# Kernel optimization log

Hardware: AMD Instinct MI355X
Metric: run time of the kernel (lower is better)

Reference implementation:

```python
import jax, jax.numpy as jnp
import numpy as np

IN_CH = 512
MID = max(IN_CH // 8, 1)


def setup_inputs() -> dict:
    key = jax.random.key(0)
    ks = jax.random.split(key, 8)
    B, C, H, W = 4, IN_CH, 64, 64
    s = 0.05
    x = jax.random.normal(ks[0], (B, C, H, W), dtype=jnp.float32)
    wq = jax.random.normal(ks[1], (MID, C), dtype=jnp.float32) * s
    bq = jnp.zeros((MID,), dtype=jnp.float32)
    wk = jax.random.normal(ks[2], (MID, C), dtype=jnp.float32) * s
    bk = jnp.zeros((MID,), dtype=jnp.float32)
    wv = jax.random.normal(ks[3], (C, C), dtype=jnp.float32) * s
    bv = jnp.zeros((C,), dtype=jnp.float32)
    alpha = jnp.ones((1,), dtype=jnp.float32) * 0.5  # nonzero so attention path is exercised
    return {"x": x, "wq": wq, "bq": bq, "wk": wk, "bk": bk, "wv": wv, "bv": bv, "alpha": alpha}


def reference(x, wq, bq, wk, bk, wv, bv, alpha):
    B, C, H, W = x.shape
    N = H * W
    xf = x.reshape(B, C, N)  # [B, C, N]
    # 1x1 convs == per-position channel GEMMs
    q = jnp.einsum('mc,bcn->bnm', wq, xf) + bq  # [B, N, mid]
    k = jnp.einsum('mc,bcn->bmn', wk, xf) + bk[None, :, None]  # [B, mid, N]
    v = jnp.einsum('dc,bcn->bdn', wv, xf) + bv[None, :, None]  # [B, C, N]
    attn = jax.nn.softmax(jnp.einsum('bnm,bmk->bnk', q, k), axis=-1)  # [B, N, N]
    out = jnp.einsum('bdn,bkn->bdk', v, attn)  # v @ attn^T -> [B, C, N]
    out = out.reshape(B, C, H, W)
    return alpha * out + x
```

## Files before the change

### kernel.cpp

```cpp
#include <hip/hip_runtime.h>

#define BB 4
#define CD 512
#define NP 4096
#define MID 64

typedef _Float16 half8 __attribute__((ext_vector_type(8)));
typedef _Float16 half4 __attribute__((ext_vector_type(4)));
typedef float floatx4 __attribute__((ext_vector_type(4)));

#define LOG2E 1.4426950408889634f

__global__ __launch_bounds__(256) void prep_w(
    const float* __restrict__ wq, const float* __restrict__ wk,
    const float* __restrict__ wv, const float* __restrict__ bq,
    const float* __restrict__ bk, const float* __restrict__ bv,
    _Float16* __restrict__ w_h, float* __restrict__ bias) {
  int idx = blockIdx.x * 256 + threadIdx.x;
  for (int i = idx; i < 640 * 512; i += gridDim.x * 256) {
    int r = i >> 9, c = i & 511;
    float v = (r < 64) ? wq[(r << 9) + c] * LOG2E
            : (r < 128) ? wk[((r - 64) << 9) + c]
                        : wv[((r - 128) << 9) + c];
    w_h[i] = (_Float16)v;
  }
  if (idx < 640) {
    float v = (idx < 64) ? bq[idx] * LOG2E
            : (idx < 128) ? bk[idx - 64]
                          : bv[idx - 128];
    bias[idx] = v;
  }
}

__global__ __launch_bounds__(256) void transpose_x(const float* __restrict__ x,
                                                   _Float16* __restrict__ xt) {
  __shared__ float tile[64][65];
  int b = blockIdx.z, c0 = blockIdx.y * 64, n0 = blockIdx.x * 64;
  int t = threadIdx.x;
  const float* xb = x + (size_t)b * CD * NP;
#pragma unroll
  for (int k = 0; k < 16; k++) {
    int cl = k * 4 + (t >> 6);
    int nl = t & 63;
    tile[cl][nl] = xb[(size_t)(c0 + cl) * NP + n0 + nl];
  }
  __syncthreads();
  _Float16* xtb = xt + ((size_t)b * NP + n0) * CD + c0;
#pragma unroll
  for (int k = 0; k < 2; k++) {
    int nl = k * 32 + (t >> 3);
    int cl = (t & 7) * 8;
    half8 pk;
#pragma unroll
    for (int i = 0; i < 8; i++) pk[i] = (_Float16)tile[cl + i][nl];
    *(half8*)(xtb + (size_t)nl * CD + cl) = pk;
  }
}

__global__ __launch_bounds__(256, 2) void proj_qkv(
    const _Float16* __restrict__ w_h, const float* __restrict__ bias,
    const _Float16* __restrict__ xt, _Float16* __restrict__ q_h,
    _Float16* __restrict__ k_h, _Float16* __restrict__ v_h) {
  __shared__ _Float16 xls[64 * 512];
  int t = threadIdx.x, w = t >> 6, lane = t & 63;
  int col = lane & 15, quad = lane >> 4;
  int rbh = blockIdx.x, nb = blockIdx.y, b = blockIdx.z;
  int n0 = nb * 64;
  const _Float16* xtb = xt + ((size_t)b * NP + n0) * CD;
#pragma unroll
  for (int j = 0; j < 16; j++) {
    int u = t + j * 256;
    int row = u >> 6, un = u & 63;
    *(half8*)(xls + row * 512 + ((un ^ (row & 7)) << 3)) =
        *(const half8*)(xtb + (size_t)row * CD + un * 8);
  }
  __syncthreads();

  int rw = rbh * 320 + w * 80;
  floatx4 acc[5][4] = {};
  for (int c = 0; c < CD; c += 32) {
    int cu = c >> 3;
    half8 a[5], bf[4];
#pragma unroll
    for (int i = 0; i < 5; i++)
      a[i] = *(const half8*)(w_h + (size_t)(rw + i * 16 + col) * CD + c + quad * 8);
#pragma unroll
    for (int j = 0; j < 4; j++) {
      int row = j * 16 + col;
      bf[j] = *(const half8*)(xls + row * 512 + (((cu + quad) ^ (row & 7)) << 3));
    }
#pragma unroll
    for (int i = 0; i < 5; i++)
#pragma unroll
      for (int j = 0; j < 4; j++)
        acc[i][j] = __builtin_amdgcn_mfma_f32_16x16x32_f16(a[i], bf[j], acc[i][j], 0, 0, 0);
  }

#pragma unroll
  for (int i = 0; i < 5; i++) {
    int r0 = rw + i * 16;
    float bi[4];
#pragma unroll
    for (int rr = 0; rr < 4; rr++) bi[rr] = bias[r0 + quad * 4 + rr];
    if (r0 < 128) {
      _Float16* dst = (r0 < 64 ? q_h + (size_t)b * NP * MID + r0
                               : k_h + (size_t)b * NP * MID + (r0 - 64));
#pragma unroll
      for (int j = 0; j < 4; j++) {
        int n = n0 + j * 16 + col;
        half4 pk;
#pragma unroll
        for (int rr = 0; rr < 4; rr++) pk[rr] = (_Float16)(acc[i][j][rr] + bi[rr]);
        *(half4*)(dst + (size_t)n * MID + quad * 4) = pk;
      }
    } else {
      int dbase = r0 - 128 + quad * 4;
#pragma unroll
      for (int j = 0; j < 4; j++) {
        int n = n0 + j * 16 + col;
#pragma unroll
        for (int rr = 0; rr < 4; rr++)
          v_h[((size_t)b * CD + dbase + rr) * NP + n] =
              (_Float16)(acc[i][j][rr] + bi[rr]);
      }
    }
  }
}

__global__ __launch_bounds__(256) void rowmax(const _Float16* __restrict__ q_h,
                                              const _Float16* __restrict__ k_h,
                                              float* __restrict__ M) {
  int qb = blockIdx.x, b = blockIdx.y;
  int t = threadIdx.x, w = t >> 6, lane = t & 63;
  int col = lane & 15, quad = lane >> 4;
  int q0 = qb * 32;
  const _Float16* qp = q_h + ((size_t)b * NP + q0) * MID;
  half8 bq[2][2];
#pragma unroll
  for (int qt = 0; qt < 2; qt++)
#pragma unroll
    for (int h = 0; h < 2; h++)
      bq[qt][h] = *(const half8*)(qp + (size_t)(qt * 16 + col) * MID + h * 32 + quad * 8);
  const _Float16* kp = k_h + ((size_t)b * NP + (size_t)w * 1024) * MID;
  float m[2] = {-1e30f, -1e30f};
#pragma unroll 4
  for (int n = 0; n < 1024; n += 16) {
    half8 ak0 = *(const half8*)(kp + (size_t)(n + col) * MID + quad * 8);
    half8 ak1 = *(const half8*)(kp + (size_t)(n + col) * MID + 32 + quad * 8);
#pragma unroll
    for (int qt = 0; qt < 2; qt++) {
      floatx4 s = {};
      s = __builtin_amdgcn_mfma_f32_16x16x32_f16(ak0, bq[qt][0], s, 0, 0, 0);
      s = __builtin_amdgcn_mfma_f32_16x16x32_f16(ak1, bq[qt][1], s, 0, 0, 0);
      m[qt] = fmaxf(m[qt], fmaxf(fmaxf(s[0], s[1]), fmaxf(s[2], s[3])));
    }
  }
  __shared__ float red[4][2][16];
#pragma unroll
  for (int qt = 0; qt < 2; qt++) {
    m[qt] = fmaxf(m[qt], __shfl_xor(m[qt], 16));
    m[qt] = fmaxf(m[qt], __shfl_xor(m[qt], 32));
  }
  if (quad == 0) {
    red[w][0][col] = m[0];
    red[w][1][col] = m[1];
  }
  __syncthreads();
  if (t < 32) {
    int qt = t >> 4, c = t & 15;
    float mm = fmaxf(fmaxf(red[0][qt][c], red[1][qt][c]),
                     fmaxf(red[2][qt][c], red[3][qt][c]));
    M[(size_t)b * NP + q0 + t] = mm;
  }
}

#define DMA16(gp, ldsoff)                                                      \
  asm volatile("s_mov_b32 m0, %0\n\t"                                         \
               "global_load_lds_dwordx4 %1, off"                              \
               :: "s"(__builtin_amdgcn_readfirstlane((int)(ldsoff))),          \
                  "v"(gp)                                                      \
               : "memory")

__global__ __launch_bounds__(256, 2) void attn_pv(
    const _Float16* __restrict__ q_h, const _Float16* __restrict__ k_h,
    const _Float16* __restrict__ v_h, const float* __restrict__ M,
    const float* __restrict__ x, const float* __restrict__ alpha_p,
    float* __restrict__ out) {
  int bid = blockIdx.x;
  int combo = bid & 7;
  int b = combo >> 1, ds = combo & 1;
  int qb = bid >> 3;
  int q0 = qb * 64, d0 = ds * 256;

  int t = threadIdx.x, w = t >> 6, lane = t & 63;
  int col = lane & 15, quad = lane >> 4;
  int c7 = col & 7;

  __shared__ floatx4 smem4[58624 / 16];
  char* smem = (char*)smem4;
  char* vbufB = smem;
  char* kbufB = smem + 32768;
  char* pbufB = smem + 40960;
  float* lred = (float*)(smem + 57344);
  float* lfin = (float*)(smem + 58368);

  const _Float16* qp = q_h + ((size_t)b * NP + q0) * MID;
  half8 bq[4][2];
#pragma unroll
  for (int qt = 0; qt < 4; qt++)
#pragma unroll
    for (int h = 0; h < 2; h++)
      bq[qt][h] = *(const half8*)(qp + (size_t)(qt * 16 + col) * MID + h * 32 + quad * 8);
  float Mq[4];
#pragma unroll
  for (int qt = 0; qt < 4; qt++) Mq[qt] = M[(size_t)b * NP + q0 + qt * 16 + col];

  int klane = (lane >> 3) * MID + (((lane & 7) ^ ((lane >> 3) & 7)) << 3);
  size_t vlane = (size_t)(lane >> 2) * NP + (((lane & 3) ^ ((lane >> 3) & 3)) << 3);

  const _Float16* kgb = k_h + (size_t)b * NP * MID;
  const _Float16* vgb = v_h + (size_t)(b * CD + d0 + w * 64) * NP;

  floatx4 acc[4][4] = {};
  float lp[4] = {0.f, 0.f, 0.f, 0.f};

  int kdw = 32768 + w * 2048;
  int vdw = w * 4096;

  int koff0 = col * 128 + ((quad ^ c7) << 4);
  int koff1 = col * 128 + (((quad ^ c7) ^ 4) << 4);
  int vswz = (quad ^ ((col >> 1) & 3)) << 4;
  int pws = ((((quad >> 1) ^ ((col >> 2) & 1)) << 4)) + ((quad & 1) << 3);
  int prs = (((quad & 1) ^ ((col >> 2) & 1)) << 4);

#pragma unroll
  for (int j = 0; j < 2; j++)
    DMA16(kgb + (size_t)(w * 16 + j * 8) * MID + klane, kdw + j * 1024);
#pragma unroll
  for (int h = 0; h < 2; h++)
#pragma unroll
    for (int j = 0; j < 4; j++)
      DMA16(vgb + (size_t)(j * 16) * NP + h * 32 + vlane,
            h * 16384 + vdw + j * 1024);

  asm volatile("s_waitcnt vmcnt(8)" ::: "memory");
  {
    const char* kb = kbufB + w * 2048;
    half8 ak0 = *(const half8*)(kb + koff0);
    half8 ak1 = *(const half8*)(kb + koff1);
    char* pbW = pbufB + w * 2048;
#pragma unroll
    for (int qt = 0; qt < 4; qt++) {
      floatx4 s = {};
      s = __builtin_amdgcn_mfma_f32_16x16x32_f16(ak0, bq[qt][0], s, 0, 0, 0);
      s = __builtin_amdgcn_mfma_f32_16x16x32_f16(ak1, bq[qt][1], s, 0, 0, 0);
      half4 pk;
#pragma unroll
      for (int r = 0; r < 4; r++) {
        float pv = __builtin_amdgcn_exp2f(s[r] - Mq[qt]);
        lp[qt] += pv;
        pk[r] = (_Float16)pv;
      }
      *(half4*)(pbW + (qt * 16 + col) * 32 + pws) = pk;
    }
    asm volatile("s_waitcnt lgkmcnt(0)" ::: "memory");
#pragma unroll
    for (int j = 0; j < 2; j++)
      DMA16(kgb + (size_t)(64 + w * 16 + j * 8) * MID + klane, kdw + j * 1024);
    asm volatile("s_barrier" ::: "memory");
  }

  for (int ci = 1; ci < 64; ci++) {
    int p = ci & 1;
    int nc = ci * 64;
    int nxt = ((ci + 1) & 63) * 64;

    asm volatile("s_waitcnt vmcnt(0)" ::: "memory");

    const char* kb = kbufB + w * 2048;
    half8 ak0 = *(const half8*)(kb + koff0);
    half8 ak1 = *(const half8*)(kb + koff1);
    const char* pbR = pbufB + (1 - p) * 8192;
    half8 bp[2][4];
#pragma unroll
    for (int h = 0; h < 2; h++)
#pragma unroll
      for (int qt = 0; qt < 4; qt++)
        bp[h][qt] = *(const half8*)(pbR + (2 * h + (quad >> 1)) * 2048 +
                                    (qt * 16 + col) * 32 + prs);
    half8 av[2][4];
#pragma unroll
    for (int h = 0; h < 2; h++)
#pragma unroll
      for (int dt = 0; dt < 4; dt++)
        av[h][dt] = *(const half8*)(vbufB + h * 16384 + vdw + dt * 1024 +
                                    col * 64 + vswz);

    floatx4 s[4];
#pragma unroll
    for (int qt = 0; qt < 4; qt++) {
      floatx4 z = {};
      z = __builtin_amdgcn_mfma_f32_16x16x32_f16(ak0, bq[qt][0], z, 0, 0, 0);
      z = __builtin_amdgcn_mfma_f32_16x16x32_f16(ak1, bq[qt][1], z, 0, 0, 0);
      s[qt] = z;
    }

    char* pbW = pbufB + p * 8192 + w * 2048;
#pragma unroll
    for (int qt = 0; qt < 4; qt++) {
      half4 pk;
#pragma unroll
      for (int r = 0; r < 4; r++) {
        float pv = __builtin_amdgcn_exp2f(s[qt][r] - Mq[qt]);
        lp[qt] += pv;
        pk[r] = (_Float16)pv;
      }
      *(half4*)(pbW + (qt * 16 + col) * 32 + pws) = pk;
    }

    asm volatile("s_waitcnt lgkmcnt(0)" ::: "memory");
#pragma unroll
    for (int j = 0; j < 2; j++)
      DMA16(kgb + (size_t)(nxt + w * 16 + j * 8) * MID + klane, kdw + j * 1024);
#pragma unroll
    for (int h = 0; h < 2; h++)
#pragma unroll
      for (int j = 0; j < 4; j++)
        DMA16(vgb + (size_t)(j * 16) * NP + nc + h * 32 + vlane,
              h * 16384 + vdw + j * 1024);

    __builtin_amdgcn_s_setprio(1);
#pragma unroll
    for (int h = 0; h < 2; h++)
#pragma unroll
      for (int dt = 0; dt < 4; dt++)
#pragma unroll
        for (int qt = 0; qt < 4; qt++)
          acc[dt][qt] = __builtin_amdgcn_mfma_f32_16x16x32_f16(
              av[h][dt], bp[h][qt], acc[dt][qt], 0, 0, 0);
    __builtin_amdgcn_s_setprio(0);

    asm volatile("s_waitcnt lgkmcnt(0)\n\ts_barrier" ::: "memory");
  }

  asm volatile("s_waitcnt vmcnt(0)" ::: "memory");
  {
    const char* pbR = pbufB + 8192;
    half8 bp[2][4];
#pragma unroll
    for (int h = 0; h < 2; h++)
#pragma unroll
      for (int qt = 0; qt < 4; qt++)
        bp[h][qt] = *(const half8*)(pbR + (2 * h + (quad >> 1)) * 2048 +
                                    (qt * 16 + col) * 32 + prs);
    half8 av[2][4];
#pragma unroll
    for (int h = 0; h < 2; h++)
#pragma unroll
      for (int dt = 0; dt < 4; dt++)
        av[h][dt] = *(const half8*)(vbufB + h * 16384 + vdw + dt * 1024 +
                                    col * 64 + vswz);
#pragma unroll
    for (int h = 0; h < 2; h++)
#pragma unroll
      for (int dt = 0; dt < 4; dt++)
#pragma unroll
        for (int qt = 0; qt < 4; qt++)
          acc[dt][qt] = __builtin_amdgcn_mfma_f32_16x16x32_f16(
              av[h][dt], bp[h][qt], acc[dt][qt], 0, 0, 0);
  }

#pragma unroll
  for (int qt = 0; qt < 4; qt++) {
    lp[qt] += __shfl_xor(lp[qt], 16);
    lp[qt] += __shfl_xor(lp[qt], 32);
    if (quad == 0) lred[(w * 4 + qt) * 16 + col] = lp[qt];
  }
  __syncthreads();
  if (t < 64) {
    int qt = t >> 4, c = t & 15;
    float l = lred[(0 + qt) * 16 + c] + lred[(4 + qt) * 16 + c] +
              lred[(8 + qt) * 16 + c] + lred[(12 + qt) * 16 + c];
    lfin[t] = alpha_p[0] / l;
  }
  __syncthreads();

  const float* xp = x + ((size_t)(b * CD + d0) + w * 64) * NP;
  float* op = out + ((size_t)(b * CD + d0) + w * 64) * NP;
#pragma unroll
  for (int dt = 0; dt < 4; dt++)
#pragma unroll
    for (int qt = 0; qt < 4; qt++) {
      float linv = lfin[qt * 16 + col];
#pragma unroll
      for (int r = 0; r < 4; r++) {
        size_t o = (size_t)(dt * 16 + quad * 4 + r) * NP + q0 + qt * 16 + col;
        op[o] = acc[dt][qt][r] * linv + xp[o];
      }
    }
}

extern "C" void kernel_launch(void* const* d_in, const int* in_sizes, int n_in,
                              void* d_out, int out_size, void* d_ws, size_t ws_size,
                              hipStream_t stream) {
  const float* x     = (const float*)d_in[0];
  const float* wq    = (const float*)d_in[1];
  const float* bq    = (const float*)d_in[2];
  const float* wk    = (const float*)d_in[3];
  const float* bk    = (const float*)d_in[4];
  const float* wv    = (const float*)d_in[5];
  const float* bv    = (const float*)d_in[6];
  const float* alpha = (const float*)d_in[7];
  float* out = (float*)d_out;

  char* ws = (char*)d_ws;
  _Float16* w_h  = (_Float16*)(ws);
  float*    bias = (float*)(ws + 655360);
  float*    Mbuf = (float*)(ws + 657920);
  _Float16* xt   = (_Float16*)(ws + 723456);
  _Float16* q_h  = (_Float16*)(ws + 17500672);
  _Float16* k_h  = (_Float16*)(ws + 19597824);
  _Float16* v_h  = (_Float16*)(ws + 21694976);

  prep_w<<<1280, 256, 0, stream>>>(wq, wk, wv, bq, bk, bv, w_h, bias);
  transpose_x<<<dim3(64, 8, BB), 256, 0, stream>>>(x, xt);
  proj_qkv<<<dim3(2, 64, BB), 256, 0, stream>>>(w_h, bias, xt, q_h, k_h, v_h);
  rowmax<<<dim3(128, BB), 256, 0, stream>>>(q_h, k_h, Mbuf);
  attn_pv<<<512, 256, 0, stream>>>(q_h, k_h, v_h, Mbuf, x, alpha, out);
}
```

Measured before the change: 255.3 us.

## Fuse weight prep with x transpose, stage V stores via LDS, reorder attn DMA

Merges the weight-conversion and x-transpose kernels into one launch to save a kernel launch and its tail. In proj_qkv the V outputs are staged through shared memory so global writes become coalesced 16-byte row stores instead of scattered 2-byte stores. In attn_pv the V tile prefetch is moved after the score MFMAs, with split waitcnts, so the K and V loads overlap differently with compute. The reordered DMA and waitcnt sequence risks exposing V load latency or causing hazards if the counts are wrong.

```diff
diff --git a/kernel.cpp b/kernel.cpp
--- a/kernel.cpp
+++ b/kernel.cpp
@@ -11,49 +11,51 @@
 
 #define LOG2E 1.4426950408889634f
 
-__global__ __launch_bounds__(256) void prep_w(
-    const float* __restrict__ wq, const float* __restrict__ wk,
-    const float* __restrict__ wv, const float* __restrict__ bq,
-    const float* __restrict__ bk, const float* __restrict__ bv,
-    _Float16* __restrict__ w_h, float* __restrict__ bias) {
-  int idx = blockIdx.x * 256 + threadIdx.x;
-  for (int i = idx; i < 640 * 512; i += gridDim.x * 256) {
-    int r = i >> 9, c = i & 511;
-    float v = (r < 64) ? wq[(r << 9) + c] * LOG2E
-            : (r < 128) ? wk[((r - 64) << 9) + c]
-                        : wv[((r - 128) << 9) + c];
-    w_h[i] = (_Float16)v;
-  }
-  if (idx < 640) {
-    float v = (idx < 64) ? bq[idx] * LOG2E
-            : (idx < 128) ? bk[idx - 64]
-                          : bv[idx - 128];
-    bias[idx] = v;
-  }
-}
-
-__global__ __launch_bounds__(256) void transpose_x(const float* __restrict__ x,
-                                                   _Float16* __restrict__ xt) {
-  __shared__ float tile[64][65];
-  int b = blockIdx.z, c0 = blockIdx.y * 64, n0 = blockIdx.x * 64;
+__global__ __launch_bounds__(256) void prep_trans(
+    const float* __restrict__ x, const float* __restrict__ wq,
+    const float* __restrict__ wk, const float* __restrict__ wv,
+    const float* __restrict__ bq, const float* __restrict__ bk,
+    const float* __restrict__ bv, _Float16* __restrict__ w_h,
+    float* __restrict__ bias, _Float16* __restrict__ xt) {
+  int bid = blockIdx.x;
   int t = threadIdx.x;
-  const float* xb = x + (size_t)b * CD * NP;
-#pragma unroll
-  for (int k = 0; k < 16; k++) {
-    int cl = k * 4 + (t >> 6);
-    int nl = t & 63;
-    tile[cl][nl] = xb[(size_t)(c0 + cl) * NP + n0 + nl];
-  }
-  __syncthreads();
-  _Float16* xtb = xt + ((size_t)b * NP + n0) * CD + c0;
-#pragma unroll
-  for (int k = 0; k < 2; k++) {
-    int nl = k * 32 + (t >> 3);
-    int cl = (t & 7) * 8;
-    half8 pk;
-#pragma unroll
-    for (int i = 0; i < 8; i++) pk[i] = (_Float16)tile[cl + i][nl];
-    *(half8*)(xtb + (size_t)nl * CD + cl) = pk;
+  if (bid < 2048) {
+    __shared__ float tile[64][65];
+    int nb = bid & 63, cb = (bid >> 6) & 7, b = bid >> 9;
+    int c0 = cb * 64, n0 = nb * 64;
+    const float* xb = x + (size_t)b * CD * NP;
+#pragma unroll
+    for (int k = 0; k < 16; k++) {
+      int cl = k * 4 + (t >> 6);
+      int nl = t & 63;
+      tile[cl][nl] = xb[(size_t)(c0 + cl) * NP + n0 + nl];
+    }
+    __syncthreads();
+    _Float16* xtb = xt + ((size_t)b * NP + n0) * CD + c0;
+#pragma unroll
+    for (int k = 0; k < 2; k++) {
+      int nl = k * 32 + (t >> 3);
+      int cl = (t & 7) * 8;
+      half8 pk;
+#pragma unroll
+      for (int i = 0; i < 8; i++) pk[i] = (_Float16)tile[cl + i][nl];
+      *(half8*)(xtb + (size_t)nl * CD + cl) = pk;
+    }
+  } else {
+    int idx = (bid - 2048) * 256 + t;
+    for (int i = idx; i < 640 * 512; i += 128 * 256) {
+      int r = i >> 9, c = i & 511;
+      float v = (r < 64) ? wq[(r << 9) + c] * LOG2E
+              : (r < 128) ? wk[((r - 64) << 9) + c]
+                          : wv[((r - 128) << 9) + c];
+      w_h[i] = (_Float16)v;
+    }
+    if (idx < 640) {
+      float v = (idx < 64) ? bq[idx] * LOG2E
+              : (idx < 128) ? bk[idx - 64]
+                            : bv[idx - 128];
+      bias[idx] = v;
+    }
   }
 }
 
@@ -96,6 +98,8 @@
         acc[i][j] = __builtin_amdgcn_mfma_f32_16x16x32_f16(a[i], bf[j], acc[i][j], 0, 0, 0);
   }
 
+  __syncthreads();
+
 #pragma unroll
   for (int i = 0; i < 5; i++) {
     int r0 = rw + i * 16;
@@ -114,16 +118,28 @@
         *(half4*)(dst + (size_t)n * MID + quad * 4) = pk;
       }
     } else {
-      int dbase = r0 - 128 + quad * 4;
+      int vl = r0 - (rbh ? 320 : 128) + quad * 4;
 #pragma unroll
       for (int j = 0; j < 4; j++) {
-        int n = n0 + j * 16 + col;
-#pragma unroll
-        for (int rr = 0; rr < 4; rr++)
-          v_h[((size_t)b * CD + dbase + rr) * NP + n] =
+#pragma unroll
+        for (int rr = 0; rr < 4; rr++) {
+          int row = vl + rr;
+          int cu2 = j * 2 + (col >> 3);
+          xls[row * 64 + ((cu2 ^ (row & 7)) << 3) + (col & 7)] =
               (_Float16)(acc[i][j][rr] + bi[rr]);
+        }
       }
     }
+  }
+  __syncthreads();
+
+  int nrows = rbh ? 320 : 192;
+  int grow0 = rbh ? 192 : 0;
+  _Float16* vdst = v_h + (size_t)b * CD * NP + n0;
+  for (int u = t; u < nrows * 8; u += 256) {
+    int row = u >> 3, un = u & 7;
+    half8 pk = *(const half8*)(xls + row * 64 + ((un ^ (row & 7)) << 3));
+    *(half8*)(vdst + (size_t)(grow0 + row) * NP + un * 8) = pk;
   }
 }
 
@@ -236,14 +252,8 @@
 #pragma unroll
   for (int j = 0; j < 2; j++)
     DMA16(kgb + (size_t)(w * 16 + j * 8) * MID + klane, kdw + j * 1024);
-#pragma unroll
-  for (int h = 0; h < 2; h++)
-#pragma unroll
-    for (int j = 0; j < 4; j++)
-      DMA16(vgb + (size_t)(j * 16) * NP + h * 32 + vlane,
-            h * 16384 + vdw + j * 1024);
-
-  asm volatile("s_waitcnt vmcnt(8)" ::: "memory");
+  asm volatile("s_waitcnt vmcnt(0)" ::: "memory");
+
   {
     const char* kb = kbufB + w * 2048;
     half8 ak0 = *(const half8*)(kb + koff0);
@@ -267,6 +277,12 @@
 #pragma unroll
     for (int j = 0; j < 2; j++)
       DMA16(kgb + (size_t)(64 + w * 16 + j * 8) * MID + klane, kdw + j * 1024);
+#pragma unroll
+    for (int h = 0; h < 2; h++)
+#pragma unroll
+      for (int j = 0; j < 4; j++)
+        DMA16(vgb + (size_t)(j * 16) * NP + h * 32 + vlane,
+              h * 16384 + vdw + j * 1024);
     asm volatile("s_barrier" ::: "memory");
   }
 
@@ -275,7 +291,7 @@
     int nc = ci * 64;
     int nxt = ((ci + 1) & 63) * 64;
 
-    asm volatile("s_waitcnt vmcnt(0)" ::: "memory");
+    asm volatile("s_waitcnt vmcnt(8)" ::: "memory");
 
     const char* kb = kbufB + w * 2048;
     half8 ak0 = *(const half8*)(kb + koff0);
@@ -288,13 +304,6 @@
       for (int qt = 0; qt < 4; qt++)
         bp[h][qt] = *(const half8*)(pbR + (2 * h + (quad >> 1)) * 2048 +
                                     (qt * 16 + col) * 32 + prs);
-    half8 av[2][4];
-#pragma unroll
-    for (int h = 0; h < 2; h++)
-#pragma unroll
-      for (int dt = 0; dt < 4; dt++)
-        av[h][dt] = *(const half8*)(vbufB + h * 16384 + vdw + dt * 1024 +
-                                    col * 64 + vswz);
 
     floatx4 s[4];
 #pragma unroll
@@ -304,6 +313,26 @@
       z = __builtin_amdgcn_mfma_f32_16x16x32_f16(ak1, bq[qt][1], z, 0, 0, 0);
       s[qt] = z;
     }
+
+    asm volatile("s_waitcnt vmcnt(0)" ::: "memory");
+    half8 av[2][4];
+#pragma unroll
+    for (int h = 0; h < 2; h++)
+#pragma unroll
+      for (int dt = 0; dt < 4; dt++)
+        av[h][dt] = *(const half8*)(vbufB + h * 16384 + vdw + dt * 1024 +
+                                    col * 64 + vswz);
+
+    asm volatile("s_waitcnt lgkmcnt(0)" ::: "memory");
+#pragma unroll
+    for (int j = 0; j < 2; j++)
+      DMA16(kgb + (size_t)(nxt + w * 16 + j * 8) * MID + klane, kdw + j * 1024);
+#pragma unroll
+    for (int h = 0; h < 2; h++)
+#pragma unroll
+      for (int j = 0; j < 4; j++)
+        DMA16(vgb + (size_t)(j * 16) * NP + nc + h * 32 + vlane,
+              h * 16384 + vdw + j * 1024);
 
     char* pbW = pbufB + p * 8192 + w * 2048;
 #pragma unroll
@@ -317,17 +346,6 @@
       }
       *(half4*)(pbW + (qt * 16 + col) * 32 + pws) = pk;
     }
-
-    asm volatile("s_waitcnt lgkmcnt(0)" ::: "memory");
-#pragma unroll
-    for (int j = 0; j < 2; j++)
-      DMA16(kgb + (size_t)(nxt + w * 16 + j * 8) * MID + klane, kdw + j * 1024);
-#pragma unroll
-    for (int h = 0; h < 2; h++)
-#pragma unroll
-      for (int j = 0; j < 4; j++)
-        DMA16(vgb + (size_t)(j * 16) * NP + nc + h * 32 + vlane,
-              h * 16384 + vdw + j * 1024);
 
     __builtin_amdgcn_s_setprio(1);
 #pragma unroll
@@ -422,8 +440,7 @@
   _Float16* k_h  = (_Float16*)(ws + 19597824);
   _Float16* v_h  = (_Float16*)(ws + 21694976);
 
-  prep_w<<<1280, 256, 0, stream>>>(wq, wk, wv, bq, bk, bv, w_h, bias);
-  transpose_x<<<dim3(64, 8, BB), 256, 0, stream>>>(x, xt);
+  prep_trans<<<2176, 256, 0, stream>>>(x, wq, wk, wv, bq, bk, bv, w_h, bias, xt);
   proj_qkv<<<dim3(2, 64, BB), 256, 0, stream>>>(w_h, bias, xt, q_h, k_h, v_h);
   rowmax<<<dim3(128, BB), 256, 0, stream>>>(q_h, k_h, Mbuf);
   attn_pv<<<512, 256, 0, stream>>>(q_h, k_h, v_h, Mbuf, x, alpha, out);
```

Result: no change. 250.4 us (-1.9%).
